# Performance work log

Measured on AMD Instinct MI355X. Metric: run time of the kernel, lower is better.

Reference implementation:

```python
import jax, jax.numpy as jnp
import numpy as np

B, T, TC, L = 128, 1024, 1024, 4
V, VT, E, H, MAX_OOV = 50000, 50000, 256, 512, 50


def setup_inputs() -> dict:
    key = jax.random.key(0)
    ks = jax.random.split(key, 20)
    s = 0.02
    emb = jax.random.normal(ks[0], (V, E), jnp.float32) * s
    emb = emb.at[0].set(0.0)  # padding_idx=0
    inp = {
        'input_ids': jax.random.randint(ks[1], (B, 1, L), 0, V),
        'h0': jax.random.normal(ks[2], (1, B, H), jnp.float32),
        'c0': jax.random.normal(ks[3], (1, B, H), jnp.float32),
        'encoder_outputs': jax.random.normal(ks[4], (B, T, H), jnp.float32),
        'context_encoder_outputs': jax.random.normal(ks[5], (B, TC, H), jnp.float32),
        'context_input': jax.random.randint(ks[6], (B, TC), 0, VT),
        'emb': emb,
        'W_ih': jax.random.normal(ks[7], (4 * H, E), jnp.float32) * s,
        'W_hh': jax.random.normal(ks[8], (4 * H, H), jnp.float32) * s,
        'b_ih': jnp.zeros((4 * H,), jnp.float32),
        'b_hh': jnp.zeros((4 * H,), jnp.float32),
        'attn_W': jax.random.normal(ks[9], (H, H), jnp.float32) * s,
        'attn_b': jnp.zeros((H,), jnp.float32),
        'cattn_W': jax.random.normal(ks[10], (H, H), jnp.float32) * s,
        'cattn_b': jnp.zeros((H,), jnp.float32),
        'gen_W': jax.random.normal(ks[11], (1, 3 * H + E), jnp.float32) * s,
        'gen_b': jnp.zeros((1,), jnp.float32),
        'sig_b': jax.random.uniform(ks[12], (1,), jnp.float32, -0.1, 0.1),
        'out_W': jax.random.normal(ks[13], (VT, H), jnp.float32) * s,
        'out_b': jnp.zeros((VT,), jnp.float32),
    }
    return inp


def reference(input_ids, h0, c0, encoder_outputs, context_encoder_outputs,
              context_input, emb, W_ih, W_hh, b_ih, b_hh, attn_W, attn_b,
              cattn_W, cattn_b, gen_W, gen_b, sig_b, out_W, out_b):
    # embed: sum subtokens, normalize by l, tanh  -> B,E (input_len == 1)
    l = input_ids.shape[2]
    x = jnp.tanh(emb[input_ids].sum(axis=2) / l)[:, 0, :]  # B,E

    # single LSTM step (PyTorch gate order i,f,g,o)
    h_prev, c_prev = h0[0], c0[0]
    gates = x @ W_ih.T + b_ih + h_prev @ W_hh.T + b_hh  # B,4H
    i, f, g, o = jnp.split(gates, 4, axis=1)
    c_new = jax.nn.sigmoid(f) * c_prev + jax.nn.sigmoid(i) * jnp.tanh(g)
    h_new = jax.nn.sigmoid(o) * jnp.tanh(c_new)
    dec = h_new  # B,H == rnn output squeezed

    # source attention (context_only)
    d1 = dec @ attn_W.T + attn_b
    scores1 = jax.nn.softmax(jnp.einsum('bth,bh->bt', encoder_outputs, d1), axis=1)
    context = jnp.einsum('bt,bth->bh', scores1, encoder_outputs)

    # context attention (score_only) + its context vector
    d2 = dec @ cattn_W.T + cattn_b
    cscores = jax.nn.softmax(jnp.einsum('bth,bh->bt', context_encoder_outputs, d2), axis=1)  # B,TC
    context_context = jnp.einsum('bt,bth->bh', cscores, context_encoder_outputs)

    # generation probability with SigmoidBias
    feat = jnp.concatenate([context, context_context, dec, x], axis=1)  # B,3H+E
    p_gen = jax.nn.sigmoid(feat @ gen_W.T + gen_b + sig_b)  # B,1
    ctx_len = (context_input > 0).sum(axis=1, keepdims=True)
    p_gen = jnp.where(ctx_len == 0, jnp.float32(1.0), p_gen)

    # vocab distribution padded with OOV zeros
    p_vocab = jax.nn.softmax(dec @ out_W.T + out_b, axis=1)
    p_vocab = jnp.concatenate([p_vocab, jnp.zeros((p_vocab.shape[0], MAX_OOV), p_vocab.dtype)], axis=1)

    # copy distribution via scatter-add of attention scores
    Bsz = dec.shape[0]
    p_copy = jnp.zeros((Bsz, VT + MAX_OOV), p_vocab.dtype)
    p_copy = p_copy.at[jnp.arange(Bsz)[:, None], context_input].add(cscores)

    out_prob = p_gen * p_vocab + (1.0 - p_gen) * p_copy
    log_prob = jnp.log(jnp.clip(out_prob, 1e-10))
    return log_prob, h_new[None], c_new[None]
```

## Files before the change

kernel.cpp:

```cpp
#include <hip/hip_runtime.h>


typedef __attribute__((ext_vector_type(8))) short short8;
typedef __attribute__((ext_vector_type(4))) float f32x4;

__device__ __forceinline__ unsigned short f2bf(float x){
  unsigned u = __float_as_uint(x);
  return (unsigned short)((u + 0x7fffu + ((u >> 16) & 1u)) >> 16);
}
__device__ __forceinline__ float sigm(float x){ return 1.f/(1.f+__expf(-x)); }

__global__ __launch_bounds__(256) void k_embed(const int* __restrict__ ids,
    const float* __restrict__ emb, const float* __restrict__ h0,
    float* __restrict__ x_f32, unsigned short* __restrict__ A_lstm){
  int b = blockIdx.x, tid = threadIdx.x;
  int i0 = ids[b*4+0], i1 = ids[b*4+1], i2 = ids[b*4+2], i3 = ids[b*4+3];
  float s = emb[(size_t)i0*256+tid] + emb[(size_t)i1*256+tid]
          + emb[(size_t)i2*256+tid] + emb[(size_t)i3*256+tid];
  float xv = tanhf(s*0.25f);
  x_f32[b*256+tid] = xv;
  A_lstm[b*768+tid] = f2bf(xv);
  for (int j = tid; j < 512; j += 256)
    A_lstm[b*768+256+j] = f2bf(h0[b*512+j]);
}

__global__ __launch_bounds__(256) void gemm128(const unsigned short* __restrict__ A, int lda,
    const float* __restrict__ Bm, const float* __restrict__ bias,
    float* __restrict__ C, int ldc, int N, int K, int addC)
{
  __shared__ unsigned short As[128*48];
  __shared__ unsigned short Bs[64*48];
  int tid = threadIdx.x, lane = tid & 63, w = tid >> 6;
  int n0 = blockIdx.x * 64;
  int mh = (w & 1) * 64, nh = (w >> 1) * 32;
  f32x4 acc[4][2];
  for (int i=0;i<4;i++) for (int j=0;j<2;j++) for (int r=0;r<4;r++) acc[i][j][r]=0.f;

  for (int k0 = 0; k0 < K; k0 += 32){
    __syncthreads();
    for (int s = tid; s < 512; s += 256){
      int row = s >> 2, ko = s & 3;
      uint4 v = *(const uint4*)(A + (size_t)row*lda + k0 + ko*8);
      *(uint4*)(&As[row*48 + ko*8]) = v;
    }
    for (int q = tid; q < 512; q += 256){
      int row = q >> 3, kq = q & 7;
      int n = n0 + row;
      float4 v = make_float4(0.f,0.f,0.f,0.f);
      if (n < N) v = *(const float4*)(Bm + (size_t)n*K + k0 + kq*4);
      unsigned p0 = (unsigned)f2bf(v.x) | ((unsigned)f2bf(v.y) << 16);
      unsigned p1 = (unsigned)f2bf(v.z) | ((unsigned)f2bf(v.w) << 16);
      *(uint2*)(&Bs[row*48 + kq*4]) = make_uint2(p0, p1);
    }
    __syncthreads();
    int kg = (lane >> 4) * 8, lr = lane & 15;
    short8 af[4], bfr[2];
    for (int i=0;i<4;i++) af[i]  = *(const short8*)(&As[(mh + i*16 + lr)*48 + kg]);
    for (int j=0;j<2;j++) bfr[j] = *(const short8*)(&Bs[(nh + j*16 + lr)*48 + kg]);
    for (int i=0;i<4;i++)
      for (int j=0;j<2;j++)
        acc[i][j] = __builtin_amdgcn_mfma_f32_16x16x32_bf16(af[i], bfr[j], acc[i][j], 0, 0, 0);
  }
  int lr = lane & 15, q4 = (lane >> 4) * 4;
  for (int i=0;i<4;i++){
    int mrow = mh + i*16 + q4;
    for (int j=0;j<2;j++){
      int n = n0 + nh + j*16 + lr;
      if (n < N){
        float bv = bias ? bias[n] : 0.f;
        for (int r=0;r<4;r++){
          float val = acc[i][j][r] + bv;
          float* p = C + (size_t)(mrow + r)*ldc + n;
          if (addC) val += *p;
          *p = val;
        }
      }
    }
  }
}

__global__ __launch_bounds__(256) void k_lstm(const float* __restrict__ gates,
    const float* __restrict__ c0, float* __restrict__ out,
    float* __restrict__ dec_f32, unsigned short* __restrict__ dec_bf){
  int idx = blockIdx.x*256 + threadIdx.x;
  int b = idx >> 9, j = idx & 511;
  const float* g = gates + (size_t)b*2048;
  float gi = g[j], gf = g[512+j], gg = g[1024+j], go = g[1536+j];
  float c = sigm(gf)*c0[idx] + sigm(gi)*tanhf(gg);
  float h = sigm(go)*tanhf(c);
  out[6406400 + idx] = h;
  out[6406400 + 65536 + idx] = c;
  dec_f32[idx] = h;
  dec_bf[idx] = f2bf(h);
}

__global__ __launch_bounds__(256) void k_attn(const float* __restrict__ enc,
    const float* __restrict__ cenc, const float* __restrict__ d1v,
    const float* __restrict__ d2v, float* __restrict__ partials,
    float* __restrict__ scraw){
  __shared__ float part[4][514];
  int chunk = blockIdx.x, b = blockIdx.y, z = blockIdx.z;
  const float* src = z ? cenc : enc;
  const float* dv  = z ? d2v : d1v;
  int tid = threadIdx.x, lane = tid & 63, w = tid >> 6;
  const float* dp = dv + b*512 + lane*8;
  float4 da = *(const float4*)dp;
  float4 db = *(const float4*)(dp+4);
  float m = -1e30f, l = 0.f;
  float acc[8];
  #pragma unroll
  for (int i=0;i<8;i++) acc[i]=0.f;
  int t0 = chunk*128 + w*32;
  for (int ti = 0; ti < 32; ti++){
    int t = t0 + ti;
    const float* row = src + ((size_t)b*1024 + t)*512 + lane*8;
    float4 va = *(const float4*)row;
    float4 vb = *(const float4*)(row+4);
    float s = va.x*da.x + va.y*da.y + va.z*da.z + va.w*da.w
            + vb.x*db.x + vb.y*db.y + vb.z*db.z + vb.w*db.w;
    #pragma unroll
    for (int off = 32; off; off >>= 1) s += __shfl_xor(s, off);
    if (z && lane == 0) scraw[b*1024 + t] = s;
    float mn = fmaxf(m, s);
    float alpha = __expf(m - mn);
    float p = __expf(s - mn);
    l = l*alpha + p; m = mn;
    acc[0]=acc[0]*alpha + p*va.x; acc[1]=acc[1]*alpha + p*va.y;
    acc[2]=acc[2]*alpha + p*va.z; acc[3]=acc[3]*alpha + p*va.w;
    acc[4]=acc[4]*alpha + p*vb.x; acc[5]=acc[5]*alpha + p*vb.y;
    acc[6]=acc[6]*alpha + p*vb.z; acc[7]=acc[7]*alpha + p*vb.w;
  }
  #pragma unroll
  for (int i=0;i<8;i++) part[w][lane*8+i] = acc[i];
  if (lane == 0){ part[w][512] = m; part[w][513] = l; }
  __syncthreads();
  float m0=part[0][512], m1=part[1][512], m2=part[2][512], m3=part[3][512];
  float ms = fmaxf(fmaxf(m0,m1), fmaxf(m2,m3));
  float e0=__expf(m0-ms), e1=__expf(m1-ms), e2=__expf(m2-ms), e3=__expf(m3-ms);
  float ls = part[0][513]*e0 + part[1][513]*e1 + part[2][513]*e2 + part[3][513]*e3;
  float* outp = partials + (size_t)((z*128 + b)*8 + chunk)*520;
  for (int j = tid; j < 512; j += 256)
    outp[j] = part[0][j]*e0 + part[1][j]*e1 + part[2][j]*e2 + part[3][j]*e3;
  if (tid == 0){ outp[512] = ms; outp[513] = ls; }
}

__global__ __launch_bounds__(256) void k_acomb(const float* __restrict__ partials,
    float* __restrict__ ctx, float* __restrict__ cctx,
    float* __restrict__ mc, float* __restrict__ lc){
  int b = blockIdx.x, z = blockIdx.y, tid = threadIdx.x;
  const float* base = partials + (size_t)((z*128 + b)*8)*520;
  float ms = -1e30f;
  for (int c=0;c<8;c++) ms = fmaxf(ms, base[c*520+512]);
  float e[8]; float ls = 0.f;
  for (int c=0;c<8;c++){ e[c] = __expf(base[c*520+512]-ms); ls += base[c*520+513]*e[c]; }
  float inv = 1.f/ls;
  float* dst = z ? cctx : ctx;
  for (int j = tid; j < 512; j += 256){
    float s = 0.f;
    for (int c=0;c<8;c++) s += base[c*520+j]*e[c];
    dst[b*512+j] = s*inv;
  }
  if (z && tid == 0){ mc[b] = ms; lc[b] = ls; }
}

__global__ __launch_bounds__(256) void k_pgen(const float* __restrict__ ctx,
    const float* __restrict__ cctx, const float* __restrict__ dec,
    const float* __restrict__ x, const float* __restrict__ genW,
    const float* __restrict__ genb, const float* __restrict__ sigb,
    const int* __restrict__ cin, float* __restrict__ pgen){
  __shared__ float sred[256]; __shared__ int cred[256];
  int b = blockIdx.x, tid = threadIdx.x;
  float p = 0.f;
  for (int j = tid; j < 1792; j += 256){
    float f = (j < 512) ? ctx[b*512+j] : (j < 1024) ? cctx[b*512+j-512]
            : (j < 1536) ? dec[b*512+j-1024] : x[b*256+j-1536];
    p += f * genW[j];
  }
  int c = 0;
  for (int t = tid; t < 1024; t += 256) c += (cin[b*1024+t] > 0);
  sred[tid] = p; cred[tid] = c; __syncthreads();
  for (int s2 = 128; s2 > 0; s2 >>= 1){
    if (tid < s2){ sred[tid] += sred[tid+s2]; cred[tid] += cred[tid+s2]; }
    __syncthreads();
  }
  if (tid == 0){
    float pg = sigm(sred[0] + genb[0] + sigb[0]);
    if (cred[0] == 0) pg = 1.f;
    pgen[b] = pg;
  }
}

__global__ __launch_bounds__(256) void k_vstats(const float* __restrict__ logits,
    float* __restrict__ mv, float* __restrict__ lv){
  __shared__ float sm[256], sl[256];
  int b = blockIdx.x, tid = threadIdx.x;
  float m = -1e30f, l = 0.f;
  const float* row = logits + (size_t)b*50000;
  for (int v = tid; v < 50000; v += 256){
    float s = row[v];
    if (s > m){ l = l*__expf(m - s) + 1.f; m = s; }
    else l += __expf(s - m);
  }
  sm[tid] = m; sl[tid] = l; __syncthreads();
  for (int s2 = 128; s2 > 0; s2 >>= 1){
    if (tid < s2){
      float m1 = sm[tid], l1 = sl[tid], m2 = sm[tid+s2], l2 = sl[tid+s2];
      float mn = fmaxf(m1, m2);
      sm[tid] = mn; sl[tid] = l1*__expf(m1-mn) + l2*__expf(m2-mn);
    }
    __syncthreads();
  }
  if (tid == 0){ mv[b] = sm[0]; lv[b] = sl[0]; }
}

__global__ __launch_bounds__(256) void k_obase(const float* __restrict__ logits,
    const float* __restrict__ mv, const float* __restrict__ lv,
    const float* __restrict__ pgen, float* __restrict__ out){
  int b = blockIdx.y;
  int v = blockIdx.x*256 + threadIdx.x;
  if (v >= 50050) return;
  float o;
  if (v < 50000){
    float pv = __expf(logits[(size_t)b*50000 + v] - mv[b]) / lv[b];
    o = logf(fmaxf(pgen[b]*pv, 1e-10f));
  } else o = -23.025850929940457f;
  out[(size_t)b*50050 + v] = o;
}

__global__ __launch_bounds__(256) void k_czero(const int* __restrict__ cin, float* __restrict__ pcopy){
  int idx = blockIdx.x*256 + threadIdx.x; int b = idx >> 10;
  pcopy[(size_t)b*50050 + cin[idx]] = 0.f;
}
__global__ __launch_bounds__(256) void k_cadd(const int* __restrict__ cin,
    const float* __restrict__ sc, const float* __restrict__ mc,
    const float* __restrict__ lc, float* __restrict__ pcopy){
  int idx = blockIdx.x*256 + threadIdx.x; int b = idx >> 10;
  float cs = __expf(sc[idx] - mc[b]) / lc[b];
  atomicAdd(&pcopy[(size_t)b*50050 + cin[idx]], cs);
}
__global__ __launch_bounds__(256) void k_cfix(const int* __restrict__ cin,
    const float* __restrict__ pcopy, const float* __restrict__ logits,
    const float* __restrict__ mv, const float* __restrict__ lv,
    const float* __restrict__ pgen, float* __restrict__ out){
  int idx = blockIdx.x*256 + threadIdx.x; int b = idx >> 10;
  int v = cin[idx];
  float pv = __expf(logits[(size_t)b*50000 + v] - mv[b]) / lv[b];
  float pg = pgen[b];
  float val = pg*pv + (1.f - pg)*pcopy[(size_t)b*50050 + v];
  out[(size_t)b*50050 + v] = logf(fmaxf(val, 1e-10f));
}

extern "C" void kernel_launch(void* const* d_in, const int* in_sizes, int n_in,
                              void* d_out, int out_size, void* d_ws, size_t ws_size,
                              hipStream_t stream){
  const int*   ids  = (const int*)d_in[0];
  const float* h0   = (const float*)d_in[1];
  const float* c0   = (const float*)d_in[2];
  const float* enc  = (const float*)d_in[3];
  const float* cenc = (const float*)d_in[4];
  const int*   cin  = (const int*)d_in[5];
  const float* emb  = (const float*)d_in[6];
  const float* Wih  = (const float*)d_in[7];
  const float* Whh  = (const float*)d_in[8];
  const float* bih  = (const float*)d_in[9];
  const float* bhh  = (const float*)d_in[10];
  const float* attW = (const float*)d_in[11];
  const float* attb = (const float*)d_in[12];
  const float* catW = (const float*)d_in[13];
  const float* catb = (const float*)d_in[14];
  const float* genW = (const float*)d_in[15];
  const float* genb = (const float*)d_in[16];
  const float* sigb = (const float*)d_in[17];
  const float* outW = (const float*)d_in[18];
  const float* outb = (const float*)d_in[19];
  float* out = (float*)d_out;
  char* ws = (char*)d_ws;

  unsigned short* A_lstm  = (unsigned short*)(ws + 0);
  float* x_f32            = (float*)(ws + 196608);
  float* gates            = (float*)(ws + 327680);
  unsigned short* dec_bf  = (unsigned short*)(ws + 1376256);
  float* dec_f32          = (float*)(ws + 1507328);
  float* d1               = (float*)(ws + 1769472);
  float* d2               = (float*)(ws + 2031616);
  float* partials         = (float*)(ws + 2293760);
  float* ctx              = (float*)(ws + 6553600);
  float* cctx             = (float*)(ws + 6815744);
  float* mc               = (float*)(ws + 7077888);
  float* lc               = (float*)(ws + 7078400);
  float* scraw            = (float*)(ws + 7078912);
  float* pgen             = (float*)(ws + 7603200);
  float* mv               = (float*)(ws + 7603712);
  float* lv               = (float*)(ws + 7604224);
  float* logits           = (float*)(ws + 7604736);
  float* pcopy            = (float*)(ws + 33204736);

  hipLaunchKernelGGL(k_embed, dim3(128), dim3(256), 0, stream, ids, emb, h0, x_f32, A_lstm);
  hipLaunchKernelGGL(gemm128, dim3(32), dim3(256), 0, stream, A_lstm,     768, Wih, bih, gates, 2048, 2048, 256, 0);
  hipLaunchKernelGGL(gemm128, dim3(32), dim3(256), 0, stream, A_lstm+256, 768, Whh, bhh, gates, 2048, 2048, 512, 1);
  hipLaunchKernelGGL(k_lstm, dim3(256), dim3(256), 0, stream, gates, c0, out, dec_f32, dec_bf);
  hipLaunchKernelGGL(gemm128, dim3(8), dim3(256), 0, stream, dec_bf, 512, attW, attb, d1, 512, 512, 512, 0);
  hipLaunchKernelGGL(gemm128, dim3(8), dim3(256), 0, stream, dec_bf, 512, catW, catb, d2, 512, 512, 512, 0);
  hipLaunchKernelGGL(gemm128, dim3(782), dim3(256), 0, stream, dec_bf, 512, outW, outb, logits, 50000, 50000, 512, 0);
  hipLaunchKernelGGL(k_attn, dim3(8,128,2), dim3(256), 0, stream, enc, cenc, d1, d2, partials, scraw);
  hipLaunchKernelGGL(k_acomb, dim3(128,2), dim3(256), 0, stream, partials, ctx, cctx, mc, lc);
  hipLaunchKernelGGL(k_pgen, dim3(128), dim3(256), 0, stream, ctx, cctx, dec_f32, x_f32, genW, genb, sigb, cin, pgen);
  hipLaunchKernelGGL(k_vstats, dim3(128), dim3(256), 0, stream, logits, mv, lv);
  hipLaunchKernelGGL(k_obase, dim3(196,128), dim3(256), 0, stream, logits, mv, lv, pgen, out);
  hipLaunchKernelGGL(k_czero, dim3(512), dim3(256), 0, stream, cin, pcopy);
  hipLaunchKernelGGL(k_cadd, dim3(512), dim3(256), 0, stream, cin, scraw, mc, lc, pcopy);
  hipLaunchKernelGGL(k_cfix, dim3(512), dim3(256), 0, stream, cin, pcopy, logits, mv, lv, pgen, out);
}
```

Baseline: 921.2 us.

## Fuse LSTM gate GEMMs with cell update, batch small GEMMs, merge copy kernels

The two gate GEMMs and the LSTM elementwise kernel become one kernel. It interleaves gate columns per block so each block computes all four gates for 16 hidden units, then applies the cell update from shared memory. The two attention projection GEMMs run as one launch, and the GEMM prefetches the next K-tile into registers. The attention combine is folded into the p_gen kernel, vocab softmax stats are split across two blocks per row, and the zero/add/fix copy kernels merge into one per-batch kernel. This cuts launches and intermediate traffic, at the cost of more register pressure and fewer blocks in some stages.

```diff
diff --git a/kernel.cpp b/kernel.cpp
--- a/kernel.cpp
+++ b/kernel.cpp
@@ -24,10 +24,94 @@
     A_lstm[b*768+256+j] = f2bf(h0[b*512+j]);
 }
 
+__global__ __launch_bounds__(256) void gemm_gates(const unsigned short* __restrict__ A,
+    const float* __restrict__ Wih, const float* __restrict__ Whh,
+    const float* __restrict__ bih, const float* __restrict__ bhh,
+    const float* __restrict__ c0, float* __restrict__ out,
+    float* __restrict__ dec_f32, unsigned short* __restrict__ dec_bf)
+{
+  __shared__ union {
+    struct { unsigned short As[128*48]; unsigned short Bs[64*48]; } s;
+    float gl[4][128][16];
+  } u;
+  int tid = threadIdx.x, lane = tid & 63, w = tid >> 6;
+  int cb = blockIdx.x * 16;
+  int mh = (w & 1) * 64, nh = (w >> 1) * 32;
+  f32x4 acc[4][2];
+  for (int i=0;i<4;i++) for (int j=0;j<2;j++) for (int r=0;r<4;r++) acc[i][j][r]=0.f;
+
+  uint4 ra[2]; float4 rb[2];
+  auto loadT = [&](int kk){
+    for (int t=0;t<2;t++){
+      int s = tid + t*256;
+      ra[t] = *(const uint4*)(A + (size_t)(s>>2)*768 + kk + (s&3)*8);
+    }
+    for (int t=0;t<2;t++){
+      int q = tid + t*256; int row = q>>3, kq = q&7;
+      int brow = (row>>4)*512 + cb + (row&15);
+      const float* p = (kk < 256) ? (Wih + (size_t)brow*256 + kk + kq*4)
+                                  : (Whh + (size_t)brow*512 + (kk-256) + kq*4);
+      rb[t] = *(const float4*)p;
+    }
+  };
+  loadT(0);
+  for (int k0 = 0; k0 < 768; k0 += 32){
+    __syncthreads();
+    for (int t=0;t<2;t++){
+      int s = tid + t*256;
+      *(uint4*)(&u.s.As[(s>>2)*48 + (s&3)*8]) = ra[t];
+    }
+    for (int t=0;t<2;t++){
+      int q = tid + t*256; int row = q>>3, kq = q&7;
+      unsigned p0 = (unsigned)f2bf(rb[t].x) | ((unsigned)f2bf(rb[t].y) << 16);
+      unsigned p1 = (unsigned)f2bf(rb[t].z) | ((unsigned)f2bf(rb[t].w) << 16);
+      *(uint2*)(&u.s.Bs[row*48 + kq*4]) = make_uint2(p0, p1);
+    }
+    __syncthreads();
+    if (k0 + 32 < 768) loadT(k0 + 32);
+    int kg = (lane >> 4) * 8, lr = lane & 15;
+    short8 af[4], bfr[2];
+    for (int i=0;i<4;i++) af[i]  = *(const short8*)(&u.s.As[(mh + i*16 + lr)*48 + kg]);
+    for (int j=0;j<2;j++) bfr[j] = *(const short8*)(&u.s.Bs[(nh + j*16 + lr)*48 + kg]);
+    for (int i=0;i<4;i++)
+      for (int j=0;j<2;j++)
+        acc[i][j] = __builtin_amdgcn_mfma_f32_16x16x32_bf16(af[i], bfr[j], acc[i][j], 0, 0, 0);
+  }
+  __syncthreads();
+  {
+    int lr = lane & 15, q4 = (lane >> 4) * 4;
+    for (int j=0;j<2;j++){
+      int nl = nh + j*16 + lr;
+      int gate = nl >> 4, c = nl & 15;
+      int brow = gate*512 + cb + c;
+      float bv = bih[brow] + bhh[brow];
+      for (int i=0;i<4;i++){
+        int m = mh + i*16 + q4;
+        for (int r=0;r<4;r++) u.gl[gate][m + r][c] = acc[i][j][r] + bv;
+      }
+    }
+  }
+  __syncthreads();
+  for (int t = tid; t < 2048; t += 256){
+    int m = t >> 4, c = t & 15, col = cb + c;
+    float gi = u.gl[0][m][c], gf = u.gl[1][m][c], gg = u.gl[2][m][c], go = u.gl[3][m][c];
+    float cc = sigm(gf)*c0[m*512+col] + sigm(gi)*tanhf(gg);
+    float h  = sigm(go)*tanhf(cc);
+    out[6406400 + m*512 + col] = h;
+    out[6406400 + 65536 + m*512 + col] = cc;
+    dec_f32[m*512+col] = h;
+    dec_bf[m*512+col] = f2bf(h);
+  }
+}
+
 __global__ __launch_bounds__(256) void gemm128(const unsigned short* __restrict__ A, int lda,
-    const float* __restrict__ Bm, const float* __restrict__ bias,
-    float* __restrict__ C, int ldc, int N, int K, int addC)
+    const float* __restrict__ B0, const float* __restrict__ bias0, float* __restrict__ C0,
+    const float* __restrict__ B1, const float* __restrict__ bias1, float* __restrict__ C1,
+    int ldc, int N, int K)
 {
+  const float* Bm  = blockIdx.y ? B1 : B0;
+  const float* bias= blockIdx.y ? bias1 : bias0;
+  float* C         = blockIdx.y ? C1 : C0;
   __shared__ unsigned short As[128*48];
   __shared__ unsigned short Bs[64*48];
   int tid = threadIdx.x, lane = tid & 63, w = tid >> 6;
@@ -36,23 +120,34 @@
   f32x4 acc[4][2];
   for (int i=0;i<4;i++) for (int j=0;j<2;j++) for (int r=0;r<4;r++) acc[i][j][r]=0.f;
 
+  uint4 ra[2]; float4 rb[2];
+  auto loadT = [&](int kk){
+    for (int t=0;t<2;t++){
+      int s = tid + t*256;
+      ra[t] = *(const uint4*)(A + (size_t)(s>>2)*lda + kk + (s&3)*8);
+    }
+    for (int t=0;t<2;t++){
+      int q = tid + t*256; int row = q>>3, kq = q&7;
+      int n = n0 + row;
+      rb[t] = (n < N) ? *(const float4*)(Bm + (size_t)n*K + kk + kq*4)
+                      : make_float4(0.f,0.f,0.f,0.f);
+    }
+  };
+  loadT(0);
   for (int k0 = 0; k0 < K; k0 += 32){
     __syncthreads();
-    for (int s = tid; s < 512; s += 256){
-      int row = s >> 2, ko = s & 3;
-      uint4 v = *(const uint4*)(A + (size_t)row*lda + k0 + ko*8);
-      *(uint4*)(&As[row*48 + ko*8]) = v;
-    }
-    for (int q = tid; q < 512; q += 256){
-      int row = q >> 3, kq = q & 7;
-      int n = n0 + row;
-      float4 v = make_float4(0.f,0.f,0.f,0.f);
-      if (n < N) v = *(const float4*)(Bm + (size_t)n*K + k0 + kq*4);
-      unsigned p0 = (unsigned)f2bf(v.x) | ((unsigned)f2bf(v.y) << 16);
-      unsigned p1 = (unsigned)f2bf(v.z) | ((unsigned)f2bf(v.w) << 16);
+    for (int t=0;t<2;t++){
+      int s = tid + t*256;
+      *(uint4*)(&As[(s>>2)*48 + (s&3)*8]) = ra[t];
+    }
+    for (int t=0;t<2;t++){
+      int q = tid + t*256; int row = q>>3, kq = q&7;
+      unsigned p0 = (unsigned)f2bf(rb[t].x) | ((unsigned)f2bf(rb[t].y) << 16);
+      unsigned p1 = (unsigned)f2bf(rb[t].z) | ((unsigned)f2bf(rb[t].w) << 16);
       *(uint2*)(&Bs[row*48 + kq*4]) = make_uint2(p0, p1);
     }
     __syncthreads();
+    if (k0 + 32 < K) loadT(k0 + 32);
     int kg = (lane >> 4) * 8, lr = lane & 15;
     short8 af[4], bfr[2];
     for (int i=0;i<4;i++) af[i]  = *(const short8*)(&As[(mh + i*16 + lr)*48 + kg]);
@@ -68,30 +163,11 @@
       int n = n0 + nh + j*16 + lr;
       if (n < N){
         float bv = bias ? bias[n] : 0.f;
-        for (int r=0;r<4;r++){
-          float val = acc[i][j][r] + bv;
-          float* p = C + (size_t)(mrow + r)*ldc + n;
-          if (addC) val += *p;
-          *p = val;
-        }
+        for (int r=0;r<4;r++)
+          C[(size_t)(mrow + r)*ldc + n] = acc[i][j][r] + bv;
       }
     }
   }
-}
-
-__global__ __launch_bounds__(256) void k_lstm(const float* __restrict__ gates,
-    const float* __restrict__ c0, float* __restrict__ out,
-    float* __restrict__ dec_f32, unsigned short* __restrict__ dec_bf){
-  int idx = blockIdx.x*256 + threadIdx.x;
-  int b = idx >> 9, j = idx & 511;
-  const float* g = gates + (size_t)b*2048;
-  float gi = g[j], gf = g[512+j], gg = g[1024+j], go = g[1536+j];
-  float c = sigm(gf)*c0[idx] + sigm(gi)*tanhf(gg);
-  float h = sigm(go)*tanhf(c);
-  out[6406400 + idx] = h;
-  out[6406400 + 65536 + idx] = c;
-  dec_f32[idx] = h;
-  dec_bf[idx] = f2bf(h);
 }
 
 __global__ __launch_bounds__(256) void k_attn(const float* __restrict__ enc,
@@ -144,38 +220,30 @@
   if (tid == 0){ outp[512] = ms; outp[513] = ls; }
 }
 
-__global__ __launch_bounds__(256) void k_acomb(const float* __restrict__ partials,
-    float* __restrict__ ctx, float* __restrict__ cctx,
-    float* __restrict__ mc, float* __restrict__ lc){
-  int b = blockIdx.x, z = blockIdx.y, tid = threadIdx.x;
-  const float* base = partials + (size_t)((z*128 + b)*8)*520;
-  float ms = -1e30f;
-  for (int c=0;c<8;c++) ms = fmaxf(ms, base[c*520+512]);
-  float e[8]; float ls = 0.f;
-  for (int c=0;c<8;c++){ e[c] = __expf(base[c*520+512]-ms); ls += base[c*520+513]*e[c]; }
-  float inv = 1.f/ls;
-  float* dst = z ? cctx : ctx;
-  for (int j = tid; j < 512; j += 256){
-    float s = 0.f;
-    for (int c=0;c<8;c++) s += base[c*520+j]*e[c];
-    dst[b*512+j] = s*inv;
-  }
-  if (z && tid == 0){ mc[b] = ms; lc[b] = ls; }
-}
-
-__global__ __launch_bounds__(256) void k_pgen(const float* __restrict__ ctx,
-    const float* __restrict__ cctx, const float* __restrict__ dec,
-    const float* __restrict__ x, const float* __restrict__ genW,
-    const float* __restrict__ genb, const float* __restrict__ sigb,
-    const int* __restrict__ cin, float* __restrict__ pgen){
+__global__ __launch_bounds__(256) void k_acomb_pgen(const float* __restrict__ partials,
+    const float* __restrict__ dec, const float* __restrict__ x,
+    const float* __restrict__ genW, const float* __restrict__ genb,
+    const float* __restrict__ sigb, const int* __restrict__ cin,
+    float* __restrict__ mc, float* __restrict__ lc, float* __restrict__ pgen){
   __shared__ float sred[256]; __shared__ int cred[256];
   int b = blockIdx.x, tid = threadIdx.x;
   float p = 0.f;
-  for (int j = tid; j < 1792; j += 256){
-    float f = (j < 512) ? ctx[b*512+j] : (j < 1024) ? cctx[b*512+j-512]
-            : (j < 1536) ? dec[b*512+j-1024] : x[b*256+j-1536];
-    p += f * genW[j];
-  }
+  for (int z = 0; z < 2; z++){
+    const float* base = partials + (size_t)((z*128 + b)*8)*520;
+    float ms = -1e30f;
+    for (int c=0;c<8;c++) ms = fmaxf(ms, base[c*520+512]);
+    float e[8]; float ls = 0.f;
+    for (int c=0;c<8;c++){ e[c] = __expf(base[c*520+512]-ms); ls += base[c*520+513]*e[c]; }
+    float inv = 1.f/ls;
+    for (int j = tid; j < 512; j += 256){
+      float s = 0.f;
+      for (int c=0;c<8;c++) s += base[c*520+j]*e[c];
+      p += s*inv*genW[z*512+j];
+    }
+    if (z == 1 && tid == 0){ mc[b] = ms; lc[b] = ls; }
+  }
+  for (int j = tid; j < 512; j += 256) p += dec[b*512+j]*genW[1024+j];
+  p += x[b*256+tid]*genW[1536+tid];
   int c = 0;
   for (int t = tid; t < 1024; t += 256) c += (cin[b*1024+t] > 0);
   sred[tid] = p; cred[tid] = c; __syncthreads();
@@ -191,12 +259,12 @@
 }
 
 __global__ __launch_bounds__(256) void k_vstats(const float* __restrict__ logits,
-    float* __restrict__ mv, float* __restrict__ lv){
+    float* __restrict__ mvp, float* __restrict__ lvp){
   __shared__ float sm[256], sl[256];
-  int b = blockIdx.x, tid = threadIdx.x;
+  int h = blockIdx.x, b = blockIdx.y, tid = threadIdx.x;
   float m = -1e30f, l = 0.f;
-  const float* row = logits + (size_t)b*50000;
-  for (int v = tid; v < 50000; v += 256){
+  const float* row = logits + (size_t)b*50000 + h*25000;
+  for (int v = tid; v < 25000; v += 256){
     float s = row[v];
     if (s > m){ l = l*__expf(m - s) + 1.f; m = s; }
     else l += __expf(s - m);
@@ -210,44 +278,59 @@
     }
     __syncthreads();
   }
-  if (tid == 0){ mv[b] = sm[0]; lv[b] = sl[0]; }
+  if (tid == 0){ mvp[b*2+h] = sm[0]; lvp[b*2+h] = sl[0]; }
 }
 
 __global__ __launch_bounds__(256) void k_obase(const float* __restrict__ logits,
-    const float* __restrict__ mv, const float* __restrict__ lv,
+    const float* __restrict__ mvp, const float* __restrict__ lvp,
     const float* __restrict__ pgen, float* __restrict__ out){
   int b = blockIdx.y;
   int v = blockIdx.x*256 + threadIdx.x;
   if (v >= 50050) return;
   float o;
   if (v < 50000){
-    float pv = __expf(logits[(size_t)b*50000 + v] - mv[b]) / lv[b];
+    float m0 = mvp[b*2], m1 = mvp[b*2+1], mm = fmaxf(m0, m1);
+    float lv = lvp[b*2]*__expf(m0-mm) + lvp[b*2+1]*__expf(m1-mm);
+    float pv = __expf(logits[(size_t)b*50000 + v] - mm) / lv;
     o = logf(fmaxf(pgen[b]*pv, 1e-10f));
   } else o = -23.025850929940457f;
   out[(size_t)b*50050 + v] = o;
 }
 
-__global__ __launch_bounds__(256) void k_czero(const int* __restrict__ cin, float* __restrict__ pcopy){
-  int idx = blockIdx.x*256 + threadIdx.x; int b = idx >> 10;
-  pcopy[(size_t)b*50050 + cin[idx]] = 0.f;
-}
-__global__ __launch_bounds__(256) void k_cadd(const int* __restrict__ cin,
-    const float* __restrict__ sc, const float* __restrict__ mc,
-    const float* __restrict__ lc, float* __restrict__ pcopy){
-  int idx = blockIdx.x*256 + threadIdx.x; int b = idx >> 10;
-  float cs = __expf(sc[idx] - mc[b]) / lc[b];
-  atomicAdd(&pcopy[(size_t)b*50050 + cin[idx]], cs);
-}
-__global__ __launch_bounds__(256) void k_cfix(const int* __restrict__ cin,
-    const float* __restrict__ pcopy, const float* __restrict__ logits,
-    const float* __restrict__ mv, const float* __restrict__ lv,
-    const float* __restrict__ pgen, float* __restrict__ out){
-  int idx = blockIdx.x*256 + threadIdx.x; int b = idx >> 10;
-  int v = cin[idx];
-  float pv = __expf(logits[(size_t)b*50000 + v] - mv[b]) / lv[b];
+__global__ __launch_bounds__(256) void k_copy(const int* __restrict__ cin,
+    const float* __restrict__ scraw, const float* __restrict__ mc,
+    const float* __restrict__ lc, const float* __restrict__ logits,
+    const float* __restrict__ mvp, const float* __restrict__ lvp,
+    const float* __restrict__ pgen, float* __restrict__ pcopy,
+    float* __restrict__ out){
+  int b = blockIdx.x, tid = threadIdx.x;
+  int vv[4];
+  #pragma unroll
+  for (int t=0;t<4;t++){
+    int idx = tid + t*256;
+    vv[t] = cin[b*1024 + idx];
+    pcopy[(size_t)b*50050 + vv[t]] = 0.f;
+  }
+  __syncthreads();
+  float mb = mc[b], lb = lc[b];
+  #pragma unroll
+  for (int t=0;t<4;t++){
+    int idx = tid + t*256;
+    float cs = __expf(scraw[b*1024 + idx] - mb) / lb;
+    atomicAdd(&pcopy[(size_t)b*50050 + vv[t]], cs);
+  }
+  __threadfence();
+  __syncthreads();
+  float m0 = mvp[b*2], m1 = mvp[b*2+1], mm = fmaxf(m0, m1);
+  float lvs = lvp[b*2]*__expf(m0-mm) + lvp[b*2+1]*__expf(m1-mm);
   float pg = pgen[b];
-  float val = pg*pv + (1.f - pg)*pcopy[(size_t)b*50050 + v];
-  out[(size_t)b*50050 + v] = logf(fmaxf(val, 1e-10f));
+  #pragma unroll
+  for (int t=0;t<4;t++){
+    int v = vv[t];
+    float pv = __expf(logits[(size_t)b*50000 + v] - mm) / lvs;
+    float val = pg*pv + (1.f - pg)*pcopy[(size_t)b*50050 + v];
+    out[(size_t)b*50050 + v] = logf(fmaxf(val, 1e-10f));
+  }
 }
 
 extern "C" void kernel_launch(void* const* d_in, const int* in_sizes, int n_in,
@@ -278,36 +361,32 @@
 
   unsigned short* A_lstm  = (unsigned short*)(ws + 0);
   float* x_f32            = (float*)(ws + 196608);
-  float* gates            = (float*)(ws + 327680);
-  unsigned short* dec_bf  = (unsigned short*)(ws + 1376256);
-  float* dec_f32          = (float*)(ws + 1507328);
-  float* d1               = (float*)(ws + 1769472);
-  float* d2               = (float*)(ws + 2031616);
-  float* partials         = (float*)(ws + 2293760);
-  float* ctx              = (float*)(ws + 6553600);
-  float* cctx             = (float*)(ws + 6815744);
-  float* mc               = (float*)(ws + 7077888);
-  float* lc               = (float*)(ws + 7078400);
-  float* scraw            = (float*)(ws + 7078912);
-  float* pgen             = (float*)(ws + 7603200);
-  float* mv               = (float*)(ws + 7603712);
-  float* lv               = (float*)(ws + 7604224);
-  float* logits           = (float*)(ws + 7604736);
-  float* pcopy            = (float*)(ws + 33204736);
+  unsigned short* dec_bf  = (unsigned short*)(ws + 327680);
+  float* dec_f32          = (float*)(ws + 458752);
+  float* d1               = (float*)(ws + 720896);
+  float* d2               = (float*)(ws + 983040);
+  float* partials         = (float*)(ws + 1245184);
+  float* mc               = (float*)(ws + 5505024);
+  float* lc               = (float*)(ws + 5505536);
+  float* scraw            = (float*)(ws + 5506048);
+  float* pgen             = (float*)(ws + 6030336);
+  float* mvp              = (float*)(ws + 6030848);
+  float* lvp              = (float*)(ws + 6031872);
+  float* logits           = (float*)(ws + 6032896);
+  float* pcopy            = (float*)(ws + 31632896);
 
   hipLaunchKernelGGL(k_embed, dim3(128), dim3(256), 0, stream, ids, emb, h0, x_f32, A_lstm);
-  hipLaunchKernelGGL(gemm128, dim3(32), dim3(256), 0, stream, A_lstm,     768, Wih, bih, gates, 2048, 2048, 256, 0);
-  hipLaunchKernelGGL(gemm128, dim3(32), dim3(256), 0, stream, A_lstm+256, 768, Whh, bhh, gates, 2048, 2048, 512, 1);
-  hipLaunchKernelGGL(k_lstm, dim3(256), dim3(256), 0, stream, gates, c0, out, dec_f32, dec_bf);
-  hipLaunchKernelGGL(gemm128, dim3(8), dim3(256), 0, stream, dec_bf, 512, attW, attb, d1, 512, 512, 512, 0);
-  hipLaunchKernelGGL(gemm128, dim3(8), dim3(256), 0, stream, dec_bf, 512, catW, catb, d2, 512, 512, 512, 0);
-  hipLaunchKernelGGL(gemm128, dim3(782), dim3(256), 0, stream, dec_bf, 512, outW, outb, logits, 50000, 50000, 512, 0);
+  hipLaunchKernelGGL(gemm_gates, dim3(32), dim3(256), 0, stream, A_lstm, Wih, Whh, bih, bhh,
+                     c0, out, dec_f32, dec_bf);
+  hipLaunchKernelGGL(gemm128, dim3(8,2), dim3(256), 0, stream, dec_bf, 512,
+                     attW, attb, d1, catW, catb, d2, 512, 512, 512);
+  hipLaunchKernelGGL(gemm128, dim3(782,1), dim3(256), 0, stream, dec_bf, 512,
+                     outW, outb, logits, outW, outb, logits, 50000, 50000, 512);
+  hipLaunchKernelGGL(k_vstats, dim3(2,128), dim3(256), 0, stream, logits, mvp, lvp);
   hipLaunchKernelGGL(k_attn, dim3(8,128,2), dim3(256), 0, stream, enc, cenc, d1, d2, partials, scraw);
-  hipLaunchKernelGGL(k_acomb, dim3(128,2), dim3(256), 0, stream, partials, ctx, cctx, mc, lc);
-  hipLaunchKernelGGL(k_pgen, dim3(128), dim3(256), 0, stream, ctx, cctx, dec_f32, x_f32, genW, genb, sigb, cin, pgen);
-  hipLaunchKernelGGL(k_vstats, dim3(128), dim3(256), 0, stream, logits, mv, lv);
-  hipLaunchKernelGGL(k_obase, dim3(196,128), dim3(256), 0, stream, logits, mv, lv, pgen, out);
-  hipLaunchKernelGGL(k_czero, dim3(512), dim3(256), 0, stream, cin, pcopy);
-  hipLaunchKernelGGL(k_cadd, dim3(512), dim3(256), 0, stream, cin, scraw, mc, lc, pcopy);
-  hipLaunchKernelGGL(k_cfix, dim3(512), dim3(256), 0, stream, cin, pcopy, logits, mv, lv, pgen, out);
-}
+  hipLaunchKernelGGL(k_acomb_pgen, dim3(128), dim3(256), 0, stream, partials, dec_f32, x_f32,
+                     genW, genb, sigb, cin, mc, lc, pgen);
+  hipLaunchKernelGGL(k_obase, dim3(196,128), dim3(256), 0, stream, logits, mvp, lvp, pgen, out);
+  hipLaunchKernelGGL(k_copy, dim3(128), dim3(256), 0, stream, cin, scraw, mc, lc, logits,
+                     mvp, lvp, pgen, pcopy, out);
+}
```

Measured after the change: 822.0 us. 1.12x faster.
